# Kernel optimization log

Measured on AMD Instinct MI355X. Metric: run time of the kernel, lower is better.

The kernel has to match this reference:

```python
import jax, jax.numpy as jnp
import numpy as np


def _hausdorff(x, y):
    # x, y: [B, C, N, D] point sets per (batch, channel); rows are points.
    x2 = jnp.sum(x * x, axis=-1)                       # [B, C, N]
    y2 = jnp.sum(y * y, axis=-1)                       # [B, C, M]
    xy = jnp.einsum('bcnd,bcmd->bcnm', x, y)           # [B, C, N, M]
    d2 = x2[..., :, None] + y2[..., None, :] - 2.0 * xy
    d = jnp.sqrt(jnp.maximum(d2, 0.0))                 # Euclidean distances
    d_fwd = jnp.max(jnp.min(d, axis=-1), axis=-1)      # max_n min_m, [B, C]
    d_bwd = jnp.max(jnp.min(d, axis=-2), axis=-1)      # max_m min_n, [B, C]
    return jnp.maximum(d_fwd, d_bwd)                   # symmetric Hausdorff [B, C]


def setup_inputs() -> dict:
    key = jax.random.key(0)
    k1, k2 = jax.random.split(key)
    B, C, H, W = 8, 3, 1024, 1024
    inp = jax.random.normal(k1, (B, C, H, W), dtype=jnp.float32)
    tgt = jax.random.normal(k2, (B, C, H, W), dtype=jnp.float32)
    return {'input': inp, 'target': tgt}


def reference(input, target):
    h = _hausdorff(input, target)        # [B, C]
    # original: sum_i mean_c(h[i]) / B == mean over (B, C)
    return jnp.mean(h)
```

## Files before the change

kernel.cpp:

```cpp
#include <hip/hip_runtime.h>
#include <math.h>

constexpr int BC = 24;
constexpr int N  = 1024;
constexpr int D  = 1024;
constexpr int TILE = 128;
constexpr int SKF = 40;

typedef short short8 __attribute__((ext_vector_type(8)));
typedef float f32x4  __attribute__((ext_vector_type(4)));
typedef long lng2    __attribute__((ext_vector_type(2)));

#define FINF 3.402823466e+38f


__device__ inline unsigned pk_bf16(float a, float b) {
    unsigned ua = __float_as_uint(a) + 0x8000u;
    unsigned ub = __float_as_uint(b) + 0x8000u;
    return __builtin_amdgcn_perm(ub, ua, 0x07060302);
}

__device__ inline int pk_fp8x4(float a, float b, float c, float d) {
    int w = __builtin_amdgcn_cvt_pk_fp8_f32(a, b, 0, false);
    w = __builtin_amdgcn_cvt_pk_fp8_f32(c, d, w, true);
    return w;
}

__global__ __launch_bounds__(256) void prep_kernel(const float* __restrict__ X,
                                                   const float* __restrict__ Y,
                                                   unsigned char* __restrict__ Xf8,
                                                   unsigned char* __restrict__ Yf8,
                                                   float* __restrict__ xn,
                                                   float* __restrict__ yn) {
    int wave = threadIdx.x >> 6, lane = threadIdx.x & 63;
    int rid0 = (blockIdx.x * 4 + wave) * 8;
    bool isY = rid0 >= 24576;
    int row0 = isY ? rid0 - 24576 : rid0;
    const float* __restrict__ src = (isY ? Y : X) + (size_t)row0 * D + lane * 4;
    unsigned char* __restrict__ dst = isY ? Yf8 : Xf8;
    float* __restrict__ nrm = isY ? yn : xn;

    int KpL   = lane >> 4;
    int inner = (((lane >> 1) & 3) << 8) | (((lane >> 3) & 1) << 3) | ((lane & 1) << 2);
    unsigned char* dbase = dst + (size_t)((row0 & ~15) + KpL) * 1024
                               + (row0 & 15) * 16 + inner;

    float4 A[4], Bv[4], Cv[4];
    #pragma unroll
    for (int q = 0; q < 4; q++) A[q]  = *(const float4*)(src + q * 256);
    #pragma unroll
    for (int q = 0; q < 4; q++) Bv[q] = *(const float4*)(src + D + q * 256);

    #pragma unroll
    for (int r = 0; r < 8; r++) {
        if (r < 6) {
            #pragma unroll
            for (int q = 0; q < 4; q++)
                Cv[q] = *(const float4*)(src + (size_t)(r + 2) * D + q * 256);
        }
        float s = 0.f;
        #pragma unroll
        for (int q = 0; q < 4; q++) {
            unsigned w = (unsigned)pk_fp8x4(A[q].x, A[q].y, A[q].z, A[q].w);
            *(unsigned*)(dbase + q * 4096 + r * 16) = w;
            s += A[q].x * A[q].x + A[q].y * A[q].y
               + A[q].z * A[q].z + A[q].w * A[q].w;
        }
        #pragma unroll
        for (int m = 1; m < 64; m <<= 1) s += __shfl_xor(s, m, 64);
        if (lane == 0) nrm[row0 + r] = s;
        #pragma unroll
        for (int q = 0; q < 4; q++) { A[q] = Bv[q]; Bv[q] = Cv[q]; }
    }
}

__global__ __launch_bounds__(256, 3) void tile_f8_kernel(const unsigned char* __restrict__ Xf8,
                                                         const unsigned char* __restrict__ Yf8,
                                                         const float* __restrict__ xn,
                                                         const float* __restrict__ yn,
                                                         unsigned* __restrict__ rowmin,
                                                         unsigned* __restrict__ colmin) {
    int id = blockIdx.x;
    int bc = id >> 6;
    int tn = (id >> 3) & 7, tm = id & 7;

    int wave = threadIdx.x >> 6, lane = threadIdx.x & 63;
    int wr = wave >> 1, wc = wave & 1;
    int quad = lane >> 4, tx = lane & 15;

    const unsigned char* Xb = Xf8 + (size_t)bc * 1024 * 1024;
    const unsigned char* Yb = Yf8 + (size_t)bc * 1024 * 1024;
    const unsigned char* ax = Xb + (size_t)(tn * 8 + wr * 4) * 16 * 1024 + lane * 16;
    const unsigned char* by = Yb + (size_t)(tm * 8 + wc * 4) * 16 * 1024 + lane * 16;

    f32x4 acc[4][4];
    #pragma unroll
    for (int i = 0; i < 4; i++)
        #pragma unroll
        for (int j = 0; j < 4; j++) acc[i][j] = (f32x4)0.f;

    lng2 a[2][4], b[2][4];
    #pragma unroll
    for (int mi = 0; mi < 4; mi++) {
        a[0][mi] = *(const lng2*)(ax + mi * 16384);
        b[0][mi] = *(const lng2*)(by + mi * 16384);
    }
    #pragma unroll
    for (int Kp = 0; Kp < 16; Kp++) {
        int cur = Kp & 1, nxt = cur ^ 1;
        if (Kp < 15) {
            #pragma unroll
            for (int mi = 0; mi < 4; mi++) {
                a[nxt][mi] = *(const lng2*)(ax + mi * 16384 + (Kp + 1) * 1024);
                b[nxt][mi] = *(const lng2*)(by + mi * 16384 + (Kp + 1) * 1024);
            }
        }
        #pragma unroll
        for (int mi = 0; mi < 4; mi++)
            #pragma unroll
            for (int mj = 0; mj < 4; mj++)
                acc[mi][mj] = __builtin_amdgcn_mfma_f32_16x16x32_fp8_fp8(a[cur][mi].x, b[cur][mj].x, acc[mi][mj], 0, 0, 0);
        #pragma unroll
        for (int mi = 0; mi < 4; mi++)
            #pragma unroll
            for (int mj = 0; mj < 4; mj++)
                acc[mi][mj] = __builtin_amdgcn_mfma_f32_16x16x32_fp8_fp8(a[cur][mi].y, b[cur][mj].y, acc[mi][mj], 0, 0, 0);
    }

    int rbase = bc * N + tn * TILE + wr * 64;
    int cbase = bc * N + tm * TILE + wc * 64;
    float xnr[4][4], ynr[4];
    #pragma unroll
    for (int mi = 0; mi < 4; mi++)
        #pragma unroll
        for (int r = 0; r < 4; r++) xnr[mi][r] = xn[rbase + mi * 16 + quad * 4 + r];
    #pragma unroll
    for (int mj = 0; mj < 4; mj++) ynr[mj] = yn[cbase + mj * 16 + tx];

    float rmin[4][4], cmin[4];
    #pragma unroll
    for (int mi = 0; mi < 4; mi++)
        #pragma unroll
        for (int r = 0; r < 4; r++) rmin[mi][r] = FINF;
    #pragma unroll
    for (int mj = 0; mj < 4; mj++) cmin[mj] = FINF;

    #pragma unroll
    for (int mi = 0; mi < 4; mi++)
        #pragma unroll
        for (int mj = 0; mj < 4; mj++)
            #pragma unroll
            for (int r = 0; r < 4; r++) {
                float d2 = fmaxf(xnr[mi][r] + ynr[mj] - 2.f * acc[mi][mj][r], 0.f);
                rmin[mi][r] = fminf(rmin[mi][r], d2);
                cmin[mj]    = fminf(cmin[mj], d2);
            }

    #pragma unroll
    for (int m = 1; m < 16; m <<= 1)
        #pragma unroll
        for (int mi = 0; mi < 4; mi++)
            #pragma unroll
            for (int r = 0; r < 4; r++)
                rmin[mi][r] = fminf(rmin[mi][r], __shfl_xor(rmin[mi][r], m, 64));
    if (tx == 0) {
        #pragma unroll
        for (int mi = 0; mi < 4; mi++)
            #pragma unroll
            for (int r = 0; r < 4; r++)
                atomicMin(&rowmin[rbase + mi * 16 + quad * 4 + r], __float_as_uint(rmin[mi][r]));
    }
    #pragma unroll
    for (int m = 16; m < 64; m <<= 1)
        #pragma unroll
        for (int mj = 0; mj < 4; mj++)
            cmin[mj] = fminf(cmin[mj], __shfl_xor(cmin[mj], m, 64));
    if (quad == 0) {
        #pragma unroll
        for (int mj = 0; mj < 4; mj++)
            atomicMin(&colmin[cbase + mj * 16 + tx], __float_as_uint(cmin[mj]));
    }
}

__global__ __launch_bounds__(256) void norms_kernel(const float* __restrict__ X,
                                                    const float* __restrict__ Y,
                                                    float* __restrict__ xn,
                                                    float* __restrict__ yn) {
    int w = threadIdx.x >> 6, lane = threadIdx.x & 63;
    long rid = (long)blockIdx.x * 4 + w;
    bool isY = rid >= (long)BC * N;
    long row = isY ? rid - (long)BC * N : rid;
    const float* src = (isY ? Y : X) + row * D;
    float s = 0.f;
    #pragma unroll
    for (int q = 0; q < 4; q++) {
        float4 v = ((const float4*)src)[lane + q * 64];
        s += v.x * v.x + v.y * v.y + v.z * v.z + v.w * v.w;
    }
    #pragma unroll
    for (int m = 1; m < 64; m <<= 1) s += __shfl_xor(s, m, 64);
    if (lane == 0) (isY ? yn : xn)[row] = s;
}

__global__ __launch_bounds__(256) void tile_conv_kernel(const float* __restrict__ X,
                                                        const float* __restrict__ Y,
                                                        const float* __restrict__ xn,
                                                        const float* __restrict__ yn,
                                                        unsigned* __restrict__ rowmin,
                                                        unsigned* __restrict__ colmin) {
    __shared__ unsigned short Xs[TILE * SKF];
    __shared__ unsigned short Ys[TILE * SKF];
    int bc = blockIdx.z, tn = blockIdx.y, tm = blockIdx.x;
    const float* Xb = X + ((size_t)bc * N + (size_t)tn * TILE) * D;
    const float* Yb = Y + ((size_t)bc * N + (size_t)tm * TILE) * D;

    int t = threadIdx.x;
    int srow = t >> 3, sq = t & 7;
    int wave = t >> 6, lane = t & 63;
    int wr = wave >> 1, wc = wave & 1;
    int quad = lane >> 4, tx = lane & 15;

    f32x4 acc[4][4];
    #pragma unroll
    for (int i = 0; i < 4; i++)
        #pragma unroll
        for (int j = 0; j < 4; j++) acc[i][j] = (f32x4)0.f;

    float4 xv[4], yv[4];
    #pragma unroll
    for (int i = 0; i < 4; i++) {
        xv[i] = *(const float4*)(Xb + (size_t)(srow + i * 32) * D + sq * 4);
        yv[i] = *(const float4*)(Yb + (size_t)(srow + i * 32) * D + sq * 4);
    }

    for (int k0 = 0; k0 < D; k0 += 32) {
        __syncthreads();
        #pragma unroll
        for (int i = 0; i < 4; i++) {
            uint2 px; px.x = pk_bf16(xv[i].x, xv[i].y); px.y = pk_bf16(xv[i].z, xv[i].w);
            *(uint2*)&Xs[(srow + i * 32) * SKF + sq * 4] = px;
            uint2 py; py.x = pk_bf16(yv[i].x, yv[i].y); py.y = pk_bf16(yv[i].z, yv[i].w);
            *(uint2*)&Ys[(srow + i * 32) * SKF + sq * 4] = py;
        }
        __syncthreads();
        if (k0 + 32 < D) {
            #pragma unroll
            for (int i = 0; i < 4; i++) {
                xv[i] = *(const float4*)(Xb + (size_t)(srow + i * 32) * D + k0 + 32 + sq * 4);
                yv[i] = *(const float4*)(Yb + (size_t)(srow + i * 32) * D + k0 + 32 + sq * 4);
            }
        }
        short8 af[4], bg[4];
        #pragma unroll
        for (int mi = 0; mi < 4; mi++)
            af[mi] = *(const short8*)&Xs[(wr * 64 + mi * 16 + tx) * SKF + quad * 8];
        #pragma unroll
        for (int mj = 0; mj < 4; mj++)
            bg[mj] = *(const short8*)&Ys[(wc * 64 + mj * 16 + tx) * SKF + quad * 8];
        #pragma unroll
        for (int mi = 0; mi < 4; mi++)
            #pragma unroll
            for (int mj = 0; mj < 4; mj++)
                acc[mi][mj] = __builtin_amdgcn_mfma_f32_16x16x32_bf16(af[mi], bg[mj], acc[mi][mj], 0, 0, 0);
    }

    int rbase = bc * N + tn * TILE + wr * 64;
    int cbase = bc * N + tm * TILE + wc * 64;
    float xnr[4][4], ynr[4];
    #pragma unroll
    for (int mi = 0; mi < 4; mi++)
        #pragma unroll
        for (int r = 0; r < 4; r++) xnr[mi][r] = xn[rbase + mi * 16 + quad * 4 + r];
    #pragma unroll
    for (int mj = 0; mj < 4; mj++) ynr[mj] = yn[cbase + mj * 16 + tx];

    float rmin[4][4], cmin[4];
    #pragma unroll
    for (int mi = 0; mi < 4; mi++)
        #pragma unroll
        for (int r = 0; r < 4; r++) rmin[mi][r] = FINF;
    #pragma unroll
    for (int mj = 0; mj < 4; mj++) cmin[mj] = FINF;

    #pragma unroll
    for (int mi = 0; mi < 4; mi++)
        #pragma unroll
        for (int mj = 0; mj < 4; mj++)
            #pragma unroll
            for (int r = 0; r < 4; r++) {
                float d2 = fmaxf(xnr[mi][r] + ynr[mj] - 2.f * acc[mi][mj][r], 0.f);
                rmin[mi][r] = fminf(rmin[mi][r], d2);
                cmin[mj]    = fminf(cmin[mj], d2);
            }

    #pragma unroll
    for (int m = 1; m < 16; m <<= 1)
        #pragma unroll
        for (int mi = 0; mi < 4; mi++)
            #pragma unroll
            for (int r = 0; r < 4; r++)
                rmin[mi][r] = fminf(rmin[mi][r], __shfl_xor(rmin[mi][r], m, 64));
    if (tx == 0) {
        #pragma unroll
        for (int mi = 0; mi < 4; mi++)
            #pragma unroll
            for (int r = 0; r < 4; r++)
                atomicMin(&rowmin[rbase + mi * 16 + quad * 4 + r], __float_as_uint(rmin[mi][r]));
    }
    #pragma unroll
    for (int m = 16; m < 64; m <<= 1)
        #pragma unroll
        for (int mj = 0; mj < 4; mj++)
            cmin[mj] = fminf(cmin[mj], __shfl_xor(cmin[mj], m, 64));
    if (quad == 0) {
        #pragma unroll
        for (int mj = 0; mj < 4; mj++)
            atomicMin(&colmin[cbase + mj * 16 + tx], __float_as_uint(cmin[mj]));
    }
}

__global__ __launch_bounds__(256) void finalize_kernel(const unsigned* __restrict__ rowmin,
                                                       const unsigned* __restrict__ colmin,
                                                       float* __restrict__ out) {
    int bc = blockIdx.x;
    float v = 0.f;
    for (int i = threadIdx.x; i < N; i += 256) {
        v = fmaxf(v, __uint_as_float(rowmin[bc * N + i]));
        v = fmaxf(v, __uint_as_float(colmin[bc * N + i]));
    }
    #pragma unroll
    for (int m = 1; m < 64; m <<= 1) v = fmaxf(v, __shfl_xor(v, m, 64));
    __shared__ float ws[4];
    int lane = threadIdx.x & 63, w = threadIdx.x >> 6;
    if (lane == 0) ws[w] = v;
    __syncthreads();
    if (threadIdx.x == 0) {
        float m = fmaxf(fmaxf(ws[0], ws[1]), fmaxf(ws[2], ws[3]));
        atomicAdd(out, sqrtf(m) * (1.0f / (float)BC));
    }
}

extern "C" void kernel_launch(void* const* d_in, const int* in_sizes, int n_in,
                              void* d_out, int out_size, void* d_ws, size_t ws_size,
                              hipStream_t stream) {
    const float* X = (const float*)d_in[0];
    const float* Y = (const float*)d_in[1];
    float* out = (float*)d_out;

    unsigned* rowmin = (unsigned*)d_ws;
    unsigned* colmin = rowmin + BC * N;
    float* xn = (float*)(colmin + BC * N);
    float* yn = xn + BC * N;
    size_t head = (size_t)4 * BC * N * 4;
    size_t f8_bytes = (size_t)BC * N * D;

    hipMemsetAsync(d_ws, 0xFF, (size_t)2 * BC * N * 4, stream);
    hipMemsetAsync(d_out, 0, sizeof(float), stream);

    if (ws_size >= head + 2 * f8_bytes) {
        unsigned char* Xf8 = (unsigned char*)d_ws + head;
        unsigned char* Yf8 = Xf8 + f8_bytes;
        prep_kernel<<<1536, 256, 0, stream>>>(X, Y, Xf8, Yf8, xn, yn);
        tile_f8_kernel<<<1536, 256, 0, stream>>>(Xf8, Yf8, xn, yn, rowmin, colmin);
    } else {
        dim3 grid(N / TILE, N / TILE, BC);
        norms_kernel<<<2 * BC * N / 4, 256, 0, stream>>>(X, Y, xn, yn);
        tile_conv_kernel<<<grid, 256, 0, stream>>>(X, Y, xn, yn, rowmin, colmin);
    }
    finalize_kernel<<<BC, 256, 0, stream>>>(rowmin, colmin, out);
}
```

Baseline: 287.2 us.

## Stage fp8 prep output through LDS for coalesced stores and remap tile block order

Result: faster. 269.7 us (-6.1%).

```diff
diff --git a/kernel.cpp b/kernel.cpp
--- a/kernel.cpp
+++ b/kernel.cpp
@@ -32,45 +32,55 @@
                                                    unsigned char* __restrict__ Yf8,
                                                    float* __restrict__ xn,
                                                    float* __restrict__ yn) {
+    __shared__ unsigned lds[16 * 260];
     int wave = threadIdx.x >> 6, lane = threadIdx.x & 63;
-    int rid0 = (blockIdx.x * 4 + wave) * 8;
-    bool isY = rid0 >= 24576;
-    int row0 = isY ? rid0 - 24576 : rid0;
-    const float* __restrict__ src = (isY ? Y : X) + (size_t)row0 * D + lane * 4;
-    unsigned char* __restrict__ dst = isY ? Yf8 : Xf8;
-    float* __restrict__ nrm = isY ? yn : xn;
-
-    int KpL   = lane >> 4;
-    int inner = (((lane >> 1) & 3) << 8) | (((lane >> 3) & 1) << 3) | ((lane & 1) << 2);
-    unsigned char* dbase = dst + (size_t)((row0 & ~15) + KpL) * 1024
-                               + (row0 & 15) * 16 + inner;
-
-    float4 A[4], Bv[4], Cv[4];
-    #pragma unroll
-    for (int q = 0; q < 4; q++) A[q]  = *(const float4*)(src + q * 256);
-    #pragma unroll
-    for (int q = 0; q < 4; q++) Bv[q] = *(const float4*)(src + D + q * 256);
-
-    #pragma unroll
-    for (int r = 0; r < 8; r++) {
-        if (r < 6) {
-            #pragma unroll
-            for (int q = 0; q < 4; q++)
-                Cv[q] = *(const float4*)(src + (size_t)(r + 2) * D + q * 256);
+    int gid = blockIdx.x;
+    bool isY = gid >= 1536;
+    int g = isY ? gid - 1536 : gid;
+    int bc = g >> 6, R = g & 63;
+
+    const float* __restrict__ src = (isY ? Y : X)
+        + ((size_t)bc * N + (size_t)R * 16 + wave * 4) * D + lane * 4;
+    unsigned char* __restrict__ dst = (isY ? Yf8 : Xf8)
+        + (size_t)(bc * 64 + R) * 16384;
+    float* __restrict__ nrm = (isY ? yn : xn) + bc * N + R * 16 + wave * 4;
+
+    float4 v[4][4];
+    #pragma unroll
+    for (int i = 0; i < 4; i++)
+        #pragma unroll
+        for (int q = 0; q < 4; q++)
+            v[i][q] = *(const float4*)(src + (size_t)i * D + q * 256);
+
+    float4 ns;
+    float* nsp = (float*)&ns;
+    #pragma unroll
+    for (int i = 0; i < 4; i++) {
+        int r = wave * 4 + i;
+        float s = 0.f;
+        #pragma unroll
+        for (int q = 0; q < 4; q++) {
+            float4 c = v[i][q];
+            lds[r * 260 + q * 64 + lane] = (unsigned)pk_fp8x4(c.x, c.y, c.z, c.w);
+            s += c.x * c.x + c.y * c.y + c.z * c.z + c.w * c.w;
         }
-        float s = 0.f;
-        #pragma unroll
-        for (int q = 0; q < 4; q++) {
-            unsigned w = (unsigned)pk_fp8x4(A[q].x, A[q].y, A[q].z, A[q].w);
-            *(unsigned*)(dbase + q * 4096 + r * 16) = w;
-            s += A[q].x * A[q].x + A[q].y * A[q].y
-               + A[q].z * A[q].z + A[q].w * A[q].w;
-        }
         #pragma unroll
         for (int m = 1; m < 64; m <<= 1) s += __shfl_xor(s, m, 64);
-        if (lane == 0) nrm[row0 + r] = s;
-        #pragma unroll
-        for (int q = 0; q < 4; q++) { A[q] = Bv[q]; Bv[q] = Cv[q]; }
+        nsp[i] = s;
+    }
+    if (lane == 0) *(float4*)nrm = ns;
+
+    __syncthreads();
+
+    int r16 = lane & 15, quad = lane >> 4;
+    #pragma unroll
+    for (int gr = 0; gr < 4; gr++) {
+        int Kp = gr * 4 + wave;
+        int di = r16 * 260 + Kp * 16 + quad * 2;
+        uint2 d0 = *(const uint2*)&lds[di];
+        uint2 d1 = *(const uint2*)&lds[di + 8];
+        uint4 w4 = make_uint4(d0.x, d0.y, d1.x, d1.y);
+        *(uint4*)(dst + Kp * 1024 + quad * 256 + r16 * 16) = w4;
     }
 }
 
@@ -80,7 +90,8 @@
                                                          const float* __restrict__ yn,
                                                          unsigned* __restrict__ rowmin,
                                                          unsigned* __restrict__ colmin) {
-    int id = blockIdx.x;
+    int raw = blockIdx.x;
+    int id = (raw & 7) * 192 + (raw >> 3);
     int bc = id >> 6;
     int tn = (id >> 3) & 7, tm = id & 7;
 
@@ -360,7 +371,7 @@
     if (ws_size >= head + 2 * f8_bytes) {
         unsigned char* Xf8 = (unsigned char*)d_ws + head;
         unsigned char* Yf8 = Xf8 + f8_bytes;
-        prep_kernel<<<1536, 256, 0, stream>>>(X, Y, Xf8, Yf8, xn, yn);
+        prep_kernel<<<3072, 256, 0, stream>>>(X, Y, Xf8, Yf8, xn, yn);
         tile_f8_kernel<<<1536, 256, 0, stream>>>(Xf8, Yf8, xn, yn, rowmin, colmin);
     } else {
         dim3 grid(N / TILE, N / TILE, BC);
```
